# Kernel optimization log

Hardware: AMD Instinct MI355X
Metric: run time of the kernel (lower is better)

Reference implementation:

```python
import jax, jax.numpy as jnp
import numpy as np

BS, QLEN, KLEN = 2, 64, 64
N_HEADS, D_KV = 8, 64
INNER = N_HEADS * D_KV  # 512
VOCAB = 4096


def _layernorm(x, g, b, eps=1e-6):
    m = jnp.mean(x, axis=-1, keepdims=True)
    v = jnp.mean(jnp.square(x - m), axis=-1, keepdims=True)
    return (x - m) * jax.lax.rsqrt(v + eps) * g + b


def _l2norm(x, eps=1e-12):
    sq = jnp.sum(jnp.square(x), axis=-1, keepdims=True)
    return x * jax.lax.rsqrt(jnp.maximum(sq, eps))


def setup_inputs() -> dict:
    key = jax.random.key(0)
    ks = jax.random.split(key, 8)
    d = {
        'query': jax.random.normal(ks[0], (BS, QLEN, INNER), jnp.float32),
        'key': jax.random.normal(ks[1], (BS, KLEN, INNER), jnp.float32),
        'q_position_embeddings': jax.random.normal(ks[2], (BS, QLEN, INNER), jnp.float32),
        'k_position_embeddings': jax.random.normal(ks[3], (BS, KLEN, INNER), jnp.float32),
        'wi_w': jax.random.normal(ks[4], (2 * INNER, INNER), jnp.float32) / np.sqrt(2 * INNER),
        'vq_dict': jax.random.normal(ks[5], (VOCAB, D_KV), jnp.float32) * np.sqrt(2.0 / (VOCAB + D_KV)),
        'vq_ln_g': jnp.ones((D_KV,), jnp.float32),
        'vq_ln_b': jnp.zeros((D_KV,), jnp.float32),
        'vq_o_w': jax.random.normal(ks[6], (D_KV, D_KV), jnp.float32) / np.sqrt(D_KV),
        'ln_g': jnp.ones((D_KV,), jnp.float32),
        'ln_b': jnp.zeros((D_KV,), jnp.float32),
    }
    return d


def reference(query, key, q_position_embeddings, k_position_embeddings,
              wi_w, vq_dict, vq_ln_g, vq_ln_b, vq_o_w, ln_g, ln_b):
    bs, qlen, dim = query.shape
    klen = key.shape[1]

    q = query + q_position_embeddings
    k = key + k_position_embeddings
    # wi(concat([q, 0])) == q @ wi_w[:dim]; wi(concat([0, k])) == k @ wi_w[dim:]
    q_proj = jnp.einsum('bqd,de->bqe', q, wi_w[:dim])   # [bs, qlen, inner]
    k_proj = jnp.einsum('bkd,de->bke', k, wi_w[dim:])   # [bs, klen, inner]

    # pairwise outer sum -> [bs, qlen, klen, inner] -> tokens of size d_kv
    rcr = q_proj[:, :, None, :] + k_proj[:, None, :, :]
    y = rcr.reshape(bs, qlen * klen * N_HEADS, D_KV)

    # --- VectorQuantizer (eval mode: no dropout, loss = 0) ---
    y_n = _l2norm(y)
    d_n = _l2norm(vq_dict)
    sim = jnp.einsum('bnd,vd->bnv', y_n, d_n)           # [bs, N, vocab]
    word_idx = jnp.argmax(sim, axis=-1)                 # [bs, N] int
    word_sim = jnp.max(sim, axis=-1)                    # [bs, N]
    z = vq_dict[word_idx]                               # gather
    emb = jax.lax.stop_gradient(z - y) + y              # straight-through
    emb = _layernorm(emb, vq_ln_g, vq_ln_b)
    emb = jnp.einsum('bnd,de->bne', emb, vq_o_w)

    r3 = emb.reshape(bs, qlen, klen, N_HEADS, D_KV)
    r3_scores = word_sim.reshape(bs, qlen, klen, N_HEADS, 1)
    out_ids = word_idx.reshape(bs, qlen, klen, N_HEADS, 1)

    r3_weighted = jnp.mean(r3 * r3_scores, axis=2)      # [bs, qlen, n_heads, d_kv]
    r3_weighted = jnp.transpose(r3_weighted, (0, 2, 1, 3))  # [bs, n_heads, qlen, d_kv]
    r3_weighted = _layernorm(r3_weighted, ln_g, ln_b)
    return r3_weighted, out_ids, r3_scores
```

## Files before the change

### kernel.cpp

```cpp
#include <hip/hip_runtime.h>
#include <math.h>

#define BS 2
#define QLEN 64
#define KLEN 64
#define NH 8
#define DKV 64
#define INNER 512
#define VOCAB 4096
#define CHUNKV 64
#define RS 130
#define BUFD (CHUNKV * RS)

typedef double vdbl4 __attribute__((ext_vector_type(4)));
typedef double vdbl2 __attribute__((ext_vector_type(2)));


__global__ __launch_bounds__(256) void k_prep(
    const float* __restrict__ q_in, const float* __restrict__ k_in,
    const float* __restrict__ qpe, const float* __restrict__ kpe,
    const float* __restrict__ wi,
    const float* __restrict__ vq, const float* __restrict__ g,
    const float* __restrict__ bta, const float* __restrict__ ow,
    double* __restrict__ qp, double* __restrict__ kp,
    double* __restrict__ dnt, float* __restrict__ E,
    unsigned long long* __restrict__ bestf)
{
    __shared__ double S[1600];
    __shared__ float Osh[4096];
    int bid = blockIdx.x;
    int t = threadIdx.x;

    if (bid < 1024) {
        int side = bid >> 9;
        int b    = (bid >> 8) & 1;
        int rp   = (bid >> 3) & 31;
        int cb   = bid & 7;
        const float* xin = side ? k_in : q_in;
        const float* pin = side ? kpe : qpe;
        double* outp = side ? kp : qp;
        int wrow0 = side ? INNER : 0;
        int r0 = rp * 2;
        double* xs = S;
        double* red = S + 1024;
        for (int i = t; i < 2 * INNER; i += 256) {
            int rr = i >> 9, dd = i & 511;
            int gidx = (b * 64 + r0 + rr) * INNER + dd;
            xs[rr * INNER + dd] = (double)xin[gidx] + (double)pin[gidx];
        }
        __syncthreads();
        int col = cb * 64 + (t & 63);
        int dh = t >> 6;
        double a0 = 0.0, a1 = 0.0;
        #pragma unroll 8
        for (int d = dh * 128; d < dh * 128 + 128; ++d) {
            double w = (double)wi[(size_t)(wrow0 + d) * INNER + col];
            a0 = fma(xs[d], w, a0);
            a1 = fma(xs[INNER + d], w, a1);
        }
        red[(dh * 2 + 0) * 64 + (t & 63)] = a0;
        red[(dh * 2 + 1) * 64 + (t & 63)] = a1;
        __syncthreads();
        if (t < 128) {
            int rr = t >> 6, c2 = t & 63;
            double s = (red[(0 * 2 + rr) * 64 + c2] + red[(1 * 2 + rr) * 64 + c2])
                     + (red[(2 * 2 + rr) * 64 + c2] + red[(3 * 2 + rr) * 64 + c2]);
            outp[(size_t)(b * 64 + r0 + rr) * INNER + cb * 64 + c2] = s;
        }
    } else {
        int db = bid - 1024;
        if (db < 256) bestf[db * 256 + t] = 0ull;
        double* Lsh = S;
        double* Dsh = S + 256;
        int vb = db * 4;
        int wv = t >> 6, lane = t & 63;
        for (int i = t; i < 4096; i += 256) Osh[i] = ow[i];
        int v = vb + wv;
        double z = (double)vq[v * DKV + lane];
        double s2 = z * z, s1 = z;
        for (int m = 32; m >= 1; m >>= 1) { s2 += __shfl_xor(s2, m); s1 += __shfl_xor(s1, m); }
        Dsh[lane * 5 + wv] = z * (1.0 / sqrt(fmax(s2, 1e-12)));
        double mean = s1 * (1.0 / 64.0);
        double d0 = z - mean;
        double vv2 = d0 * d0;
        for (int m = 32; m >= 1; m >>= 1) vv2 += __shfl_xor(vv2, m);
        vv2 *= (1.0 / 64.0);
        Lsh[wv * 64 + lane] = d0 * (1.0 / sqrt(vv2 + 1e-6)) * (double)g[lane] + (double)bta[lane];
        __syncthreads();
        double c0 = 0.0, c1 = 0.0, c2 = 0.0, c3 = 0.0;
        #pragma unroll 4
        for (int gg = 0; gg < 16; ++gg) {
            int jj = gg * 4;
            c0 = fma(Lsh[wv * 64 + jj + 0], (double)Osh[(jj + 0) * 64 + lane], c0);
            c1 = fma(Lsh[wv * 64 + jj + 1], (double)Osh[(jj + 1) * 64 + lane], c1);
            c2 = fma(Lsh[wv * 64 + jj + 2], (double)Osh[(jj + 2) * 64 + lane], c2);
            c3 = fma(Lsh[wv * 64 + jj + 3], (double)Osh[(jj + 3) * 64 + lane], c3);
        }
        E[v * DKV + lane] = (float)((c0 + c1) + (c2 + c3));
        {
            int j = t >> 2, vloc = t & 3;
            dnt[(size_t)j * VOCAB + vb + vloc] = Dsh[j * 5 + vloc];
        }
    }
}

__global__ __launch_bounds__(1024, 4) void k_simscan(
    const double* __restrict__ qp, const double* __restrict__ kp,
    const double* __restrict__ dnt,
    unsigned long long* __restrict__ bestf)
{
    int bid = blockIdx.x;
    int bh = bid & 15, cg = bid >> 4;
    int b = bh >> 3, h = bh & 7;
    int t = threadIdx.x;
    int w = t >> 6, l = t & 63;

    __shared__ double S[2 * BUFD];
    __shared__ int sem[9];

    int asub = l >> 4;
    int lrow = l & 15;
    bool isprod = (w < 8);

    if (t < 9) sem[t] = 0;

    int drow[4], dcol[4];
    {
        vdbl4 prow = (vdbl4){0.0, 0.0, 0.0, 0.0};
        vdbl4 pcol = (vdbl4){0.0, 0.0, 0.0, 0.0};
        double a_row = (asub == 0) ? (double)lrow : 0.0;
        double b_one = (asub == 0) ? 1.0 : 0.0;
        double a_one = (asub == 0) ? 1.0 : 0.0;
        double b_col = (asub == 0) ? (double)lrow : 0.0;
        prow = __builtin_amdgcn_mfma_f64_16x16x4f64(a_row, b_one, prow, 0, 0, 0);
        pcol = __builtin_amdgcn_mfma_f64_16x16x4f64(a_one, b_col, pcol, 0, 0, 0);
        #pragma unroll
        for (int r = 0; r < 4; ++r) { drow[r] = (int)prow[r]; dcol[r] = (int)pcol[r]; }
    }

    double afr[16];
    if (isprod) {
        const double* src = (w < 4) ? qp : kp;
        int arow = (w & 3) * 16 + lrow;
        #pragma unroll
        for (int ks = 0; ks < 16; ++ks)
            afr[ks] = src[(size_t)(b * 64 + arow) * INNER + h * 64 + ks * 4 + asub];
    }

    int ci = t - 512;
    int qi = ci & 7;
    int kb = (ci >> 3) & 15;
    int vs = ci >> 7;
    int qo[4];
    #pragma unroll
    for (int r = 0; r < 4; ++r) qo[r] = (4 * qi + ((r + qi) & 3)) * 2;
    int ko0 = 64 + 4 * kb;
    double best[8][4];
    #pragma unroll
    for (int a = 0; a < 8; ++a)
        #pragma unroll
        for (int b2 = 0; b2 < 4; ++b2) best[a][b2] = 0.0;

    __syncthreads();

    if (isprod) {
        for (int step = 0; step < 4; ++step) {
            if (step >= 2) {
                for (;;) {
                    int c0 = 0;
                    if (l == 0) c0 = atomicAdd(&sem[4 + step - 2], 0);
                    if (__shfl(c0, 0) >= 8) break;
                    __builtin_amdgcn_s_sleep(2);
                }
            }
            int v0 = (cg * 4 + step) * CHUNKV;
            double* buf = S + (step & 1) * BUFD;
            vdbl4 acc[4];
            #pragma unroll
            for (int vt = 0; vt < 4; ++vt) acc[vt] = (vdbl4){0.0, 0.0, 0.0, 0.0};
            size_t base = (size_t)asub * VOCAB + v0 + lrow;
            double bcur[4], bnext[4];
            #pragma unroll
            for (int vt = 0; vt < 4; ++vt) bcur[vt] = dnt[base + vt * 16];
            #pragma unroll
            for (int ks = 0; ks < 16; ++ks) {
                if (ks < 15) {
                    size_t krow = base + (size_t)((ks + 1) * 4) * VOCAB;
                    #pragma unroll
                    for (int vt = 0; vt < 4; ++vt) bnext[vt] = dnt[krow + vt * 16];
                }
                #pragma unroll
                for (int vt = 0; vt < 4; ++vt)
                    acc[vt] = __builtin_amdgcn_mfma_f64_16x16x4f64(
                        afr[ks], bcur[vt], acc[vt], 0, 0, 0);
                if (ks < 15) {
                    #pragma unroll
                    for (int vt = 0; vt < 4; ++vt) bcur[vt] = bnext[vt];
                }
            }
            bool isq = (w < 4);
            #pragma unroll
            for (int vt = 0; vt < 4; ++vt)
                #pragma unroll
                for (int r = 0; r < 4; ++r) {
                    int vl = vt * 16 + dcol[r];
                    int grow = (w & 3) * 16 + drow[r];
                    int slot;
                    if (isq) {
                        int qi8 = grow >> 3, rr = (grow >> 1) & 3;
                        slot = (4 * qi8 + ((rr + qi8) & 3)) * 2 + (grow & 1);
                    } else {
                        slot = 64 + grow;
                    }
                    unsigned long long code =
                        (unsigned long long)((4095 - (v0 + vl)) << 1);
                    double s = fma(acc[vt][r], 1.0 / 64.0, 1.5);
                    unsigned long long bb2 = __double_as_longlong(s) & ~0x1FFFull;
                    if (isq) bb2 |= code;
                    buf[vl * RS + slot] = __longlong_as_double(bb2);
                }
            __threadfence_block();
            if (l == 0) atomicAdd(&sem[step], 1);
        }
    } else {
        for (int step = 0; step < 4; ++step) {
            for (;;) {
                int c0 = 0;
                if (l == 0) c0 = atomicAdd(&sem[step], 0);
                if (__shfl(c0, 0) >= 8) break;
                __builtin_amdgcn_s_sleep(2);
            }
            const double* row = S + (step & 1) * BUFD + vs * 16 * RS;
            #pragma unroll 2
            for (int vi = 0; vi < 16; ++vi, row += RS) {
                vdbl2 q0 = *(const vdbl2*)(row + qo[0]);
                vdbl2 q1 = *(const vdbl2*)(row + qo[1]);
                vdbl2 q2 = *(const vdbl2*)(row + qo[2]);
                vdbl2 q3 = *(const vdbl2*)(row + qo[3]);
                vdbl2 k0 = *(const vdbl2*)(row + ko0);
                vdbl2 k1 = *(const vdbl2*)(row + ko0 + 2);
                double qa[8] = {q0[0], q0[1], q1[0], q1[1],
                                q2[0], q2[1], q3[0], q3[1]};
                double kv0 = k0[0], kv1 = k0[1], kv2 = k1[0], kv3 = k1[1];
                #pragma unroll
                for (int a = 0; a < 8; ++a) {
                    best[a][0] = fmax(best[a][0], qa[a] + kv0);
                    best[a][1] = fmax(best[a][1], qa[a] + kv1);
                    best[a][2] = fmax(best[a][2], qa[a] + kv2);
                    best[a][3] = fmax(best[a][3], qa[a] + kv3);
                }
            }
            __threadfence_block();
            if (l == 0) atomicAdd(&sem[4 + step], 1);
        }
        for (;;) {
            int c0 = 0;
            if (l == 0) c0 = atomicAdd(&sem[7], 0);
            if (__shfl(c0, 0) >= 8) break;
            __builtin_amdgcn_s_sleep(2);
        }
        double* red = S;
        #pragma unroll
        for (int a = 0; a < 8; ++a)
            #pragma unroll
            for (int b2 = 0; b2 < 4; ++b2)
                red[(a * 4 + b2) * 512 + ci] = best[a][b2];
        __threadfence_block();
        if (l == 0) atomicAdd(&sem[8], 1);
        if (ci < 128) {
            for (;;) {
                int c0 = 0;
                if (l == 0) c0 = atomicAdd(&sem[8], 0);
                if (__shfl(c0, 0) >= 8) break;
                __builtin_amdgcn_s_sleep(2);
            }
            #pragma unroll
            for (int j = 0; j < 32; ++j) {
                double m0 = fmax(red[j * 512 + ci], red[j * 512 + ci + 128]);
                double m1 = fmax(red[j * 512 + ci + 256], red[j * 512 + ci + 384]);
                double m = fmax(m0, m1);
                int q = qi * 8 + (j >> 2);
                int k = kb * 4 + (j & 3);
                atomicMax(&bestf[((size_t)bh * 64 + q) * 64 + k],
                          (unsigned long long)__double_as_longlong(m));
            }
        }
    }
}

__global__ __launch_bounds__(256) void k_combine(
    const unsigned long long* __restrict__ bestf,
    const double* __restrict__ qp, const double* __restrict__ kp,
    const float* __restrict__ E,
    const float* __restrict__ lng, const float* __restrict__ lnb,
    float* __restrict__ out)
{
    int bid = blockIdx.x;
    int bh = bid & 15, q = bid >> 4;
    int b = bh >> 3, h = bh & 7;
    int t = threadIdx.x;
    int w = t >> 6, lane = t & 63;

    __shared__ double qrow[64];
    __shared__ double gpart[4][64];
    __shared__ double knpart[4][64];
    __shared__ double qnpart[4];
    __shared__ float  ws_l[64];
    __shared__ int    idx_l[64];
    __shared__ float  epart[4][64];

    if (t < 64) qrow[t] = qp[(size_t)(b * 64 + q) * INNER + h * 64 + t];
    __syncthreads();

    {
        const double* krow = kp + (size_t)(b * 64 + lane) * INNER + h * 64 + w * 16;
        double gd = 0.0, kn = 0.0;
        #pragma unroll
        for (int i = 0; i < 16; ++i) {
            double xk = krow[i];
            gd = fma(qrow[w * 16 + i], xk, gd);
            kn = fma(xk, xk, kn);
        }
        gpart[w][lane] = gd;
        knpart[w][lane] = kn;
        if (lane == 0) {
            double qn = 0.0;
            #pragma unroll
            for (int i = 0; i < 16; ++i) { double xq = qrow[w * 16 + i]; qn = fma(xq, xq, qn); }
            qnpart[w] = qn;
        }
    }
    __syncthreads();

    if (w == 0) {
        int k = lane;
        double gdot = (gpart[0][k] + gpart[1][k]) + (gpart[2][k] + gpart[3][k]);
        double kn2  = (knpart[0][k] + knpart[1][k]) + (knpart[2][k] + knpart[3][k]);
        double qn2  = (qnpart[0] + qnpart[1]) + (qnpart[2] + qnpart[3]);
        unsigned long long bb = bestf[((size_t)bh * 64 + q) * 64 + k];
        int vidx = 4095 - (int)(bb & 0xFFFull);
        double sval = __longlong_as_double(bb & ~0x1FFFull);
        double tru = (sval - 3.0) * 64.0;
        double n2 = qn2 + kn2 + 2.0 * gdot;
        double wsim = tru * (1.0 / sqrt(fmax(n2, 1e-12)));
        size_t oidx = ((size_t)(b * QLEN + q) * KLEN + k) * NH + h;
        out[65536 + oidx] = (float)vidx;
        out[131072 + oidx] = (float)wsim;
        ws_l[k] = (float)wsim;
        idx_l[k] = vidx;
    }
    __syncthreads();

    {
        int d = lane;
        float acc = 0.0f;
        #pragma unroll 4
        for (int k2 = w * 16; k2 < w * 16 + 16; ++k2)
            acc += E[idx_l[k2] * DKV + d] * ws_l[k2];
        epart[w][d] = acc;
    }
    __syncthreads();

    if (w == 0) {
        int d = lane;
        float acc = ((epart[0][d] + epart[1][d]) + (epart[2][d] + epart[3][d])) * (1.0f / 64.0f);
        float mean = acc;
        for (int m = 32; m >= 1; m >>= 1) mean += __shfl_xor(mean, m);
        mean *= (1.0f / 64.0f);
        float dv = acc - mean;
        float var = dv * dv;
        for (int m = 32; m >= 1; m >>= 1) var += __shfl_xor(var, m);
        var *= (1.0f / 64.0f);
        float o = dv * rsqrtf(var + 1e-6f) * lng[d] + lnb[d];
        out[(((size_t)b * NH + h) * QLEN + q) * DKV + d] = o;
    }
}

extern "C" void kernel_launch(void* const* d_in, const int* in_sizes, int n_in,
                              void* d_out, int out_size, void* d_ws, size_t ws_size,
                              hipStream_t stream) {
    const float* query = (const float*)d_in[0];
    const float* key   = (const float*)d_in[1];
    const float* qpe   = (const float*)d_in[2];
    const float* kpe   = (const float*)d_in[3];
    const float* wi    = (const float*)d_in[4];
    const float* vq    = (const float*)d_in[5];
    const float* vqg   = (const float*)d_in[6];
    const float* vqb   = (const float*)d_in[7];
    const float* ow    = (const float*)d_in[8];
    const float* lng   = (const float*)d_in[9];
    const float* lnb   = (const float*)d_in[10];
    float* out = (float*)d_out;

    char* ws = (char*)d_ws;
    double* qp  = (double*)(ws + 0);
    double* kp  = (double*)(ws + 524288);
    double* dnt = (double*)(ws + 1048576);
    float*  E   = (float*) (ws + 3145728);
    unsigned long long* bestf = (unsigned long long*)(ws + 4194304);

    k_prep   <<<2048, 256, 0, stream>>>(query, key, qpe, kpe, wi, vq, vqg, vqb, ow,
                                        qp, kp, dnt, E, bestf);
    k_simscan<<<256, 1024, 0, stream>>>(qp, kp, dnt, bestf);
    k_combine<<<1024, 256, 0, stream>>>(bestf, qp, kp, E, lng, lnb, out);
}
```

Baseline: 168.7 us.

## Retile consumer max-reduction to 4x4 tiles with vec4 LDS loads

The consumer warps now each own a 4q x 4k register tile over 32 vocab rows, instead of an 8q x 4k tile over 16 rows. Q scores are stored contiguously in the shared buffer, so each row needs two 32-byte vector loads. The swizzled slot layout goes away. The final reduction becomes a two-way exchange between vocab halves in place of a four-way LDS reduction, which halves register state and reduction traffic. In exchange, there are fewer FMAs per load and possible LDS bank conflicts from the unswizzled contiguous layout.

```diff
diff --git a/kernel.cpp b/kernel.cpp
--- a/kernel.cpp
+++ b/kernel.cpp
@@ -148,16 +148,12 @@
     }
 
     int ci = t - 512;
-    int qi = ci & 7;
-    int kb = (ci >> 3) & 15;
-    int vs = ci >> 7;
-    int qo[4];
+    int qi = ci & 15;
+    int kb = (ci >> 4) & 15;
+    int vs = ci >> 8;
+    double best[4][4];
     #pragma unroll
-    for (int r = 0; r < 4; ++r) qo[r] = (4 * qi + ((r + qi) & 3)) * 2;
-    int ko0 = 64 + 4 * kb;
-    double best[8][4];
-    #pragma unroll
-    for (int a = 0; a < 8; ++a)
+    for (int a = 0; a < 4; ++a)
         #pragma unroll
         for (int b2 = 0; b2 < 4; ++b2) best[a][b2] = 0.0;
 
@@ -205,13 +201,7 @@
                 for (int r = 0; r < 4; ++r) {
                     int vl = vt * 16 + dcol[r];
                     int grow = (w & 3) * 16 + drow[r];
-                    int slot;
-                    if (isq) {
-                        int qi8 = grow >> 3, rr = (grow >> 1) & 3;
-                        slot = (4 * qi8 + ((rr + qi8) & 3)) * 2 + (grow & 1);
-                    } else {
-                        slot = 64 + grow;
-                    }
+                    int slot = isq ? grow : (64 + grow);
                     unsigned long long code =
                         (unsigned long long)((4095 - (v0 + vl)) << 1);
                     double s = fma(acc[vt][r], 1.0 / 64.0, 1.5);
@@ -230,24 +220,17 @@
                 if (__shfl(c0, 0) >= 8) break;
                 __builtin_amdgcn_s_sleep(2);
             }
-            const double* row = S + (step & 1) * BUFD + vs * 16 * RS;
+            const double* row = S + (step & 1) * BUFD + (size_t)vs * 32 * RS;
             #pragma unroll 2
-            for (int vi = 0; vi < 16; ++vi, row += RS) {
-                vdbl2 q0 = *(const vdbl2*)(row + qo[0]);
-                vdbl2 q1 = *(const vdbl2*)(row + qo[1]);
-                vdbl2 q2 = *(const vdbl2*)(row + qo[2]);
-                vdbl2 q3 = *(const vdbl2*)(row + qo[3]);
-                vdbl2 k0 = *(const vdbl2*)(row + ko0);
-                vdbl2 k1 = *(const vdbl2*)(row + ko0 + 2);
-                double qa[8] = {q0[0], q0[1], q1[0], q1[1],
-                                q2[0], q2[1], q3[0], q3[1]};
-                double kv0 = k0[0], kv1 = k0[1], kv2 = k1[0], kv3 = k1[1];
+            for (int vi = 0; vi < 32; ++vi, row += RS) {
+                vdbl4 qv = *(const vdbl4*)(row + qi * 4);
+                vdbl4 kv = *(const vdbl4*)(row + 64 + kb * 4);
                 #pragma unroll
-                for (int a = 0; a < 8; ++a) {
-                    best[a][0] = fmax(best[a][0], qa[a] + kv0);
-                    best[a][1] = fmax(best[a][1], qa[a] + kv1);
-                    best[a][2] = fmax(best[a][2], qa[a] + kv2);
-                    best[a][3] = fmax(best[a][3], qa[a] + kv3);
+                for (int a = 0; a < 4; ++a) {
+                    best[a][0] = fmax(best[a][0], qv[a] + kv[0]);
+                    best[a][1] = fmax(best[a][1], qv[a] + kv[1]);
+                    best[a][2] = fmax(best[a][2], qv[a] + kv[2]);
+                    best[a][3] = fmax(best[a][3], qv[a] + kv[3]);
                 }
             }
             __threadfence_block();
@@ -260,26 +243,24 @@
             __builtin_amdgcn_s_sleep(2);
         }
         double* red = S;
-        #pragma unroll
-        for (int a = 0; a < 8; ++a)
-            #pragma unroll
-            for (int b2 = 0; b2 < 4; ++b2)
-                red[(a * 4 + b2) * 512 + ci] = best[a][b2];
-        __threadfence_block();
-        if (l == 0) atomicAdd(&sem[8], 1);
-        if (ci < 128) {
+        if (vs == 0) {
+            #pragma unroll
+            for (int j = 0; j < 16; ++j)
+                red[j * 256 + ci] = best[j >> 2][j & 3];
+            __threadfence_block();
+            if (l == 0) atomicAdd(&sem[8], 1);
+        } else {
             for (;;) {
                 int c0 = 0;
                 if (l == 0) c0 = atomicAdd(&sem[8], 0);
-                if (__shfl(c0, 0) >= 8) break;
+                if (__shfl(c0, 0) >= 4) break;
                 __builtin_amdgcn_s_sleep(2);
             }
-            #pragma unroll
-            for (int j = 0; j < 32; ++j) {
-                double m0 = fmax(red[j * 512 + ci], red[j * 512 + ci + 128]);
-                double m1 = fmax(red[j * 512 + ci + 256], red[j * 512 + ci + 384]);
-                double m = fmax(m0, m1);
-                int q = qi * 8 + (j >> 2);
+            int cib = ci - 256;
+            #pragma unroll
+            for (int j = 0; j < 16; ++j) {
+                double m = fmax(best[j >> 2][j & 3], red[j * 256 + cib]);
+                int q = qi * 4 + (j >> 2);
                 int k = kb * 4 + (j & 3);
                 atomicMax(&bestf[((size_t)bh * 64 + q) * 64 + k],
                           (unsigned long long)__double_as_longlong(m));
```

Measured after the change: 167.5 us. About the same (-0.7%).
